# Optimization experiments

Hardware: AMD Instinct MI355X
Metric: run time of the kernel (lower is better)

## Reference

```python
import jax, jax.numpy as jnp
import numpy as np
import math

N_HEADS = 8
Q_DIM = 512          # number of query tokens (first Q_DIM rows of q)
INPUT_DIM = 512
EMBED_DIM = 512
HEAD_DIM = EMBED_DIM // N_HEADS  # key_dim == val_dim == 64
BATCH = 8
TOTAL_TOKENS = 4096  # Q_DIM queries + 3584 context tokens
NORM = 1.0 / math.sqrt(HEAD_DIM)


def setup_inputs() -> dict:
    key = jax.random.key(0)
    k1, k2, k3, k4, k5 = jax.random.split(key, 5)
    stdv = 1.0 / math.sqrt(HEAD_DIM)
    return {
        "q": jax.random.normal(k1, (BATCH, TOTAL_TOKENS, INPUT_DIM), dtype=jnp.float32),
        "W_query": jax.random.uniform(k2, (N_HEADS, INPUT_DIM, HEAD_DIM), minval=-stdv, maxval=stdv, dtype=jnp.float32),
        "W_key": jax.random.uniform(k3, (N_HEADS, INPUT_DIM, HEAD_DIM), minval=-stdv, maxval=stdv, dtype=jnp.float32),
        "W_val": jax.random.uniform(k4, (N_HEADS, INPUT_DIM, HEAD_DIM), minval=-stdv, maxval=stdv, dtype=jnp.float32),
        "W_out": jax.random.uniform(k5, (N_HEADS, HEAD_DIM, EMBED_DIM), minval=-1.0 / math.sqrt(EMBED_DIM), maxval=1.0 / math.sqrt(EMBED_DIM), dtype=jnp.float32),
    }


def reference(q, W_query, W_key, W_val, W_out):
    # Split packed input: first Q_DIM tokens are queries, rest are context.
    q_ = q[:, :Q_DIM, :]          # [b, nq, d_in]
    h = q[:, Q_DIM:, :]           # [b, g, d_in]
    Q = jnp.einsum('bqi,hik->hbqk', q_, W_query)   # [h, b, nq, dk]
    K = jnp.einsum('bgi,hik->hbgk', h, W_key)      # [h, b, g, dk]
    V = jnp.einsum('bgi,hiv->hbgv', h, W_val)      # [h, b, g, dv]
    compat = NORM * jnp.einsum('hbqk,hbgk->hbqg', Q, K)  # [h, b, nq, g]
    attn = jax.nn.softmax(compat, axis=-1)
    heads = jnp.einsum('hbqg,hbgv->hbqv', attn, V)       # [h, b, nq, dv]
    out = jnp.einsum('hbqv,hve->bqe', heads, W_out)      # [b, nq, embed]
    return out
```

## Files before the change

### kernel.cpp

```cpp
#include <hip/hip_runtime.h>

typedef _Float16 f16;
typedef _Float16 f16x4 __attribute__((ext_vector_type(4)));
typedef _Float16 f16x8 __attribute__((ext_vector_type(8)));
typedef float    f32x4 __attribute__((ext_vector_type(4)));

#define MFMA(a,b,c) __builtin_amdgcn_mfma_f32_16x16x32_f16(a,b,c,0,0,0)

__device__ __forceinline__ void gld16(const void* g, void* l) {
  typedef __attribute__((address_space(1))) unsigned GU;
  typedef __attribute__((address_space(3))) unsigned LU;
  __builtin_amdgcn_global_load_lds((GU*)g, (LU*)l, 16, 0, 0);
}

__global__ __launch_bounds__(256) void conv_w(
    const float* __restrict__ Wq, const float* __restrict__ Wk,
    const float* __restrict__ Wv, const float* __restrict__ Wo,
    f16* __restrict__ Wqt, f16* __restrict__ Wkt, f16* __restrict__ Wvt,
    f16* __restrict__ Wot)
{
  int idx = blockIdx.x * 256 + threadIdx.x;
  int c = idx & 511, i = idx >> 9;
  int h = c >> 6, k = c & 63;
  int src = (h * 512 + i) * 64 + k;
  Wqt[c * 512 + i] = (f16)(Wq[src] * 0.125f);
  Wkt[c * 512 + i] = (f16)Wk[src];
  Wvt[c * 512 + i] = (f16)Wv[src];
  Wot[idx] = (f16)Wo[(idx & 511) * 512 + (idx >> 9)];
}

__global__ __launch_bounds__(256) void proj_kernel(
    const float* __restrict__ q,
    const f16* __restrict__ Wqt, const f16* __restrict__ Wkt, const f16* __restrict__ Wvt,
    f16* __restrict__ Qh, f16* __restrict__ Kh, f16* __restrict__ Vtb)
{
  __shared__ f16 Asl[2][4096];
  __shared__ f16 Bsl[2][4096];

  int bid = blockIdx.x;
  int mode, t;
  if (bid < 128)       { mode = 0; t = bid; }
  else if (bid < 1024) { mode = 1; t = bid - 128; }
  else                 { mode = 2; t = bid - 1024; }
  int rt = t >> 2, ct = t & 3;
  const f16* Wt = (mode == 0) ? Wqt : (mode == 1) ? Wkt : Wvt;

  int tid = threadIdx.x, l = tid & 63, w = tid >> 6;
  int m0 = rt * 128, n0 = ct * 128;
  int wr = w >> 1, wc = w & 1;

  int arl = tid >> 3;
  int acol = (tid & 7) * 4;
  int agrow[4], awb[4];
#pragma unroll
  for (int p = 0; p < 4; ++p) {
    int m = m0 + p * 32 + arl;
    int grow;
    if (mode == 0) grow = (m >> 9) * 4096 + (m & 511);
    else { int b = m / 3584; grow = b * 4096 + 512 + (m - b * 3584); }
    agrow[p] = grow * 512;
    int r = p * 32 + arl, cg = tid & 7;
    awb[p] = r * 64 + (((cg >> 1) ^ (r & 3)) << 4) + (cg & 1) * 8;
  }
  int bn[2], bco[2];
#pragma unroll
  for (int j = 0; j < 2; ++j) {
    int n = (w * 2 + j) * 16 + (l >> 2);
    bn[j] = n;
    bco[j] = ((l & 3) ^ (n & 3)) * 8;
  }

  const f32x4 z4 = {0.f, 0.f, 0.f, 0.f};
  f32x4 acc[4][4];
#pragma unroll
  for (int i = 0; i < 4; ++i)
#pragma unroll
    for (int jj = 0; jj < 4; ++jj) acc[i][jj] = z4;

  f32x4 areg[4];
  auto aload = [&](int k0) {
#pragma unroll
    for (int p = 0; p < 4; ++p)
      areg[p] = *(const f32x4*)(q + agrow[p] + k0 + acol);
  };
  auto bstage = [&](int bufi, int k0) {
#pragma unroll
    for (int j = 0; j < 2; ++j)
      gld16(Wt + (n0 + bn[j]) * 512 + k0 + bco[j], &Bsl[bufi][(w * 2 + j) * 512]);
  };
  auto awrite = [&](int bufi) {
#pragma unroll
    for (int p = 0; p < 4; ++p) {
      f16x4 h4;
      h4[0] = (f16)areg[p][0]; h4[1] = (f16)areg[p][1];
      h4[2] = (f16)areg[p][2]; h4[3] = (f16)areg[p][3];
      *(f16x4*)((char*)&Asl[bufi][0] + awb[p]) = h4;
    }
  };

  aload(0); bstage(0, 0); awrite(0);
  __syncthreads();

  for (int ks = 0; ks < 16; ++ks) {
    int bufi = ks & 1;
    if (ks < 15) { aload((ks + 1) * 32); bstage(bufi ^ 1, (ks + 1) * 32); }
    const char* AB = (const char*)&Asl[bufi][0];
    const char* BB = (const char*)&Bsl[bufi][0];
    f16x8 af[4], bf[4];
#pragma unroll
    for (int mi = 0; mi < 4; ++mi) {
      int row = wr * 64 + mi * 16 + (l & 15);
      af[mi] = *(const f16x8*)(AB + row * 64 + (((l >> 4) ^ (row & 3)) << 4));
    }
#pragma unroll
    for (int ni = 0; ni < 4; ++ni) {
      int rn = wc * 64 + ni * 16 + (l & 15);
      bf[ni] = *(const f16x8*)(BB + rn * 64 + (((l >> 4) ^ (rn & 3)) << 4));
    }
#pragma unroll
    for (int mi = 0; mi < 4; ++mi)
#pragma unroll
      for (int ni = 0; ni < 4; ++ni)
        acc[mi][ni] = MFMA(af[mi], bf[ni], acc[mi][ni]);
    if (ks < 15) awrite(bufi ^ 1);
    __syncthreads();
  }

  if (mode < 2) {
    f16* Out = (mode == 0) ? Qh : Kh;
#pragma unroll
    for (int mi = 0; mi < 4; ++mi) {
      int row = m0 + wr * 64 + mi * 16 + (l >> 4) * 4;
#pragma unroll
      for (int ni = 0; ni < 4; ++ni) {
        int col = n0 + wc * 64 + ni * 16 + (l & 15);
#pragma unroll
        for (int r = 0; r < 4; ++r)
          Out[(row + r) * 512 + col] = (f16)acc[mi][ni][r];
      }
    }
  } else {
#pragma unroll
    for (int mi = 0; mi < 4; ++mi) {
      int m = m0 + wr * 64 + mi * 16 + (l >> 4) * 4;
      int b = m / 3584, g = m - b * 3584;
#pragma unroll
      for (int ni = 0; ni < 4; ++ni) {
        int c = n0 + wc * 64 + ni * 16 + (l & 15);
        int hh = c >> 6, v = c & 63;
        f16x4 o4;
        o4[0] = (f16)acc[mi][ni][0]; o4[1] = (f16)acc[mi][ni][1];
        o4[2] = (f16)acc[mi][ni][2]; o4[3] = (f16)acc[mi][ni][3];
        *(f16x4*)(Vtb + ((b * 8 + hh) * 64 + v) * 3584 + g) = o4;
      }
    }
  }
}

__global__ __launch_bounds__(512) void attn_kernel(
    const f16* __restrict__ Qh, const f16* __restrict__ Kh,
    const f16* __restrict__ Vtb, f16* __restrict__ Hm)
{
  __shared__ f16 Klds[2][4096];
  __shared__ f16 Vlds[2][4096];
  __shared__ f16 Plds[8192];

  int bid = blockIdx.x;
  int qt = bid & 3, h = (bid >> 2) & 7, bb = bid >> 5;
  int q0 = qt * 128;
  int tid = threadIdx.x, l = tid & 63, w = tid >> 6;

  f16x8 qf0, qf1;
  {
    int qrow = q0 + w * 16 + (l & 15);
    const f16* qb = Qh + (bb * 512 + qrow) * 512 + h * 64 + ((l >> 4) * 8);
    qf0 = *(const f16x8*)qb;
    qf1 = *(const f16x8*)(qb + 32);
  }

  bool isK = (w < 4);
  int sdo[2], ssrc[2];
#pragma unroll
  for (int j = 0; j < 2; ++j) {
    int id = (isK ? w : (w - 4)) * 2 + j;
    int rr = id * 8 + (l >> 3);
    int co = ((l & 7) ^ (rr & 7)) * 8;
    sdo[j] = id * 512;
    if (isK) ssrc[j] = (bb * 3584 + rr) * 512 + h * 64 + co;
    else     ssrc[j] = ((bb * 8 + h) * 64 + rr) * 3584 + co;
  }

  const f32x4 z4 = {0.f, 0.f, 0.f, 0.f};
  f32x4 acco[4];
#pragma unroll
  for (int i = 0; i < 4; ++i) acco[i] = z4;
  float mrow[4], lrow[4];
#pragma unroll
  for (int r = 0; r < 4; ++r) { mrow[r] = -1e30f; lrow[r] = 0.f; }

  char* PwB = (char*)&Plds[w * 1024];

  if (isK) { gld16(Kh + ssrc[0], &Klds[0][sdo[0]]); gld16(Kh + ssrc[1], &Klds[0][sdo[1]]); }
  else     { gld16(Vtb + ssrc[0], &Vlds[0][sdo[0]]); gld16(Vtb + ssrc[1], &Vlds[0][sdo[1]]); }
  __syncthreads();

  int buf = 0;
  for (int it = 0; it < 56; ++it) {
    if (it < 55) {
      int g0 = (it + 1) * 64;
      if (isK) { gld16(Kh + ssrc[0] + g0 * 512, &Klds[buf ^ 1][sdo[0]]);
                 gld16(Kh + ssrc[1] + g0 * 512, &Klds[buf ^ 1][sdo[1]]); }
      else     { gld16(Vtb + ssrc[0] + g0, &Vlds[buf ^ 1][sdo[0]]);
                 gld16(Vtb + ssrc[1] + g0, &Vlds[buf ^ 1][sdo[1]]); }
    }
    const char* KB = (const char*)&Klds[buf][0];
    const char* VB = (const char*)&Vlds[buf][0];

    f32x4 accs[4];
#pragma unroll
    for (int i = 0; i < 4; ++i) accs[i] = z4;
#pragma unroll
    for (int ni = 0; ni < 4; ++ni) {
      int g = ni * 16 + (l & 15);
      f16x8 kb0 = *(const f16x8*)(KB + g * 128 + ((((l >> 4)    ) ^ (g & 7)) << 4));
      f16x8 kb1 = *(const f16x8*)(KB + g * 128 + (((4 + (l >> 4)) ^ (g & 7)) << 4));
      accs[ni] = MFMA(qf0, kb0, accs[ni]);
      accs[ni] = MFMA(qf1, kb1, accs[ni]);
    }

    float alpha[4];
#pragma unroll
    for (int r = 0; r < 4; ++r) {
      float tm = fmaxf(fmaxf(accs[0][r], accs[1][r]), fmaxf(accs[2][r], accs[3][r]));
      tm = fmaxf(tm, __shfl_xor(tm, 1));
      tm = fmaxf(tm, __shfl_xor(tm, 2));
      tm = fmaxf(tm, __shfl_xor(tm, 4));
      tm = fmaxf(tm, __shfl_xor(tm, 8));
      float mn = fmaxf(mrow[r], tm);
      alpha[r] = __expf(mrow[r] - mn);
      mrow[r] = mn;
    }
    float rsum[4] = {0.f, 0.f, 0.f, 0.f};
    int qbase = (l >> 4) * 4;
#pragma unroll
    for (int ni = 0; ni < 4; ++ni) {
      int g = ni * 16 + (l & 15);
#pragma unroll
      for (int r = 0; r < 4; ++r) {
        float p = __expf(accs[ni][r] - mrow[r]);
        rsum[r] += p;
        int qq = qbase + r;
        *(f16*)(PwB + qq * 128 + ((((g >> 3) ^ (qq & 7))) << 4) + (g & 7) * 2) = (f16)p;
      }
    }
#pragma unroll
    for (int r = 0; r < 4; ++r) {
      rsum[r] += __shfl_xor(rsum[r], 1);
      rsum[r] += __shfl_xor(rsum[r], 2);
      rsum[r] += __shfl_xor(rsum[r], 4);
      rsum[r] += __shfl_xor(rsum[r], 8);
      lrow[r] = lrow[r] * alpha[r] + rsum[r];
    }
#pragma unroll
    for (int ni = 0; ni < 4; ++ni)
#pragma unroll
      for (int r = 0; r < 4; ++r) acco[ni][r] *= alpha[r];

    asm volatile("s_waitcnt lgkmcnt(0)" ::: "memory");

#pragma unroll
    for (int kc = 0; kc < 2; ++kc) {
      int qq = l & 15;
      int ch = kc * 4 + (l >> 4);
      f16x8 pa = *(const f16x8*)(PwB + qq * 128 + ((ch ^ (qq & 7)) << 4));
#pragma unroll
      for (int ni = 0; ni < 4; ++ni) {
        int v = ni * 16 + (l & 15);
        f16x8 vb = *(const f16x8*)(VB + v * 128 + ((ch ^ (v & 7)) << 4));
        acco[ni] = MFMA(pa, vb, acco[ni]);
      }
    }

    __syncthreads();
    buf ^= 1;
  }

#pragma unroll
  for (int r = 0; r < 4; ++r) {
    float inv = 1.f / lrow[r];
    int qrow = q0 + w * 16 + (l >> 4) * 4 + r;
    f16* ob = Hm + (bb * 512 + qrow) * 512 + h * 64 + (l & 15);
#pragma unroll
    for (int ni = 0; ni < 4; ++ni)
      ob[ni * 16] = (f16)(acco[ni][r] * inv);
  }
}

__global__ __launch_bounds__(256) void outproj_kernel(
    const f16* __restrict__ Hm, const f16* __restrict__ Wot, float* __restrict__ out)
{
  __shared__ f16 Asl[2][4096];
  __shared__ f16 Bsl[2][4096];
  int bid = blockIdx.x;
  int rt = bid >> 2, ct = bid & 3;
  int tid = threadIdx.x, l = tid & 63, w = tid >> 6;
  int m0 = rt * 128, n0 = ct * 128;
  int wr = w >> 1, wc = w & 1;

  int an[2], aco[2];
#pragma unroll
  for (int j = 0; j < 2; ++j) {
    int r = (w * 2 + j) * 16 + (l >> 2);
    an[j] = r;
    aco[j] = ((l & 3) ^ (r & 3)) * 8;
  }

  const f32x4 z4 = {0.f, 0.f, 0.f, 0.f};
  f32x4 acc[4][4];
#pragma unroll
  for (int i = 0; i < 4; ++i)
#pragma unroll
    for (int jj = 0; jj < 4; ++jj) acc[i][jj] = z4;

  auto stage = [&](int bufi, int k0) {
#pragma unroll
    for (int j = 0; j < 2; ++j) {
      gld16(Hm  + (m0 + an[j]) * 512 + k0 + aco[j], &Asl[bufi][(w * 2 + j) * 512]);
      gld16(Wot + (n0 + an[j]) * 512 + k0 + aco[j], &Bsl[bufi][(w * 2 + j) * 512]);
    }
  };

  stage(0, 0);
  __syncthreads();
  for (int ks = 0; ks < 16; ++ks) {
    int bufi = ks & 1;
    if (ks < 15) stage(bufi ^ 1, (ks + 1) * 32);
    const char* AB = (const char*)&Asl[bufi][0];
    const char* BB = (const char*)&Bsl[bufi][0];
    f16x8 af[4], bf[4];
#pragma unroll
    for (int mi = 0; mi < 4; ++mi) {
      int row = wr * 64 + mi * 16 + (l & 15);
      af[mi] = *(const f16x8*)(AB + row * 64 + (((l >> 4) ^ (row & 3)) << 4));
    }
#pragma unroll
    for (int ni = 0; ni < 4; ++ni) {
      int rn = wc * 64 + ni * 16 + (l & 15);
      bf[ni] = *(const f16x8*)(BB + rn * 64 + (((l >> 4) ^ (rn & 3)) << 4));
    }
#pragma unroll
    for (int mi = 0; mi < 4; ++mi)
#pragma unroll
      for (int ni = 0; ni < 4; ++ni)
        acc[mi][ni] = MFMA(af[mi], bf[ni], acc[mi][ni]);
    __syncthreads();
  }

#pragma unroll
  for (int mi = 0; mi < 4; ++mi) {
    int row = m0 + wr * 64 + mi * 16 + (l >> 4) * 4;
#pragma unroll
    for (int ni = 0; ni < 4; ++ni) {
      int col = n0 + wc * 64 + ni * 16 + (l & 15);
#pragma unroll
      for (int r = 0; r < 4; ++r)
        out[(row + r) * 512 + col] = acc[mi][ni][r];
    }
  }
}

extern "C" void kernel_launch(void* const* d_in, const int* in_sizes, int n_in,
                              void* d_out, int out_size, void* d_ws, size_t ws_size,
                              hipStream_t stream) {
  const float* q  = (const float*)d_in[0];
  const float* Wq = (const float*)d_in[1];
  const float* Wk = (const float*)d_in[2];
  const float* Wv = (const float*)d_in[3];
  const float* Wo = (const float*)d_in[4];
  float* out = (float*)d_out;

  f16* ws  = (f16*)d_ws;
  f16* Wqt = ws;
  f16* Wkt = Wqt + 262144;
  f16* Wvt = Wkt + 262144;
  f16* Wot = Wvt + 262144;
  f16* Qh  = Wot + 262144;
  f16* Kh  = Qh  + 4096 * 512;
  f16* Vtb = Kh  + 28672 * 512;
  f16* Hm  = Vtb + 28672 * 512;

  conv_w<<<dim3(1024), dim3(256), 0, stream>>>(Wq, Wk, Wv, Wo, Wqt, Wkt, Wvt, Wot);
  proj_kernel<<<dim3(1920), dim3(256), 0, stream>>>(q, Wqt, Wkt, Wvt, Qh, Kh, Vtb);
  attn_kernel<<<dim3(256), dim3(512), 0, stream>>>(Qh, Kh, Vtb, Hm);
  outproj_kernel<<<dim3(128), dim3(256), 0, stream>>>(Hm, Wot, out);
}
```

Before: 284.8 us.

## Split attention over two KV segments with merge kernel, exp2 softmax, tiled weight transpose

The attention kernel now splits the 3584 context tokens into two halves per block, doubling the grid to 512 blocks, and writes partial outputs plus row max and sum. A new merge kernel combines them. The change also swaps the MFMA operand order so each lane owns a single query row, which cuts cross-lane reductions. It uses exp2 with log2(e) folded into the query weights, and replaces the weight conversion with an LDS-tiled transpose. The goal is better CU occupancy on a 256-CU part and cheaper softmax, at the cost of an extra kernel launch and extra partial-output memory traffic.

```diff
diff --git a/kernel.cpp b/kernel.cpp
--- a/kernel.cpp
+++ b/kernel.cpp
@@ -7,26 +7,51 @@
 
 #define MFMA(a,b,c) __builtin_amdgcn_mfma_f32_16x16x32_f16(a,b,c,0,0,0)
 
+#if __has_builtin(__builtin_amdgcn_exp2f)
+#define EXP2(x) __builtin_amdgcn_exp2f(x)
+#else
+#define EXP2(x) exp2f(x)
+#endif
+
 __device__ __forceinline__ void gld16(const void* g, void* l) {
   typedef __attribute__((address_space(1))) unsigned GU;
   typedef __attribute__((address_space(3))) unsigned LU;
   __builtin_amdgcn_global_load_lds((GU*)g, (LU*)l, 16, 0, 0);
 }
 
-__global__ __launch_bounds__(256) void conv_w(
+__global__ __launch_bounds__(256) void transp_w(
     const float* __restrict__ Wq, const float* __restrict__ Wk,
     const float* __restrict__ Wv, const float* __restrict__ Wo,
     f16* __restrict__ Wqt, f16* __restrict__ Wkt, f16* __restrict__ Wvt,
     f16* __restrict__ Wot)
 {
-  int idx = blockIdx.x * 256 + threadIdx.x;
-  int c = idx & 511, i = idx >> 9;
-  int h = c >> 6, k = c & 63;
-  int src = (h * 512 + i) * 64 + k;
-  Wqt[c * 512 + i] = (f16)(Wq[src] * 0.125f);
-  Wkt[c * 512 + i] = (f16)Wk[src];
-  Wvt[c * 512 + i] = (f16)Wv[src];
-  Wot[idx] = (f16)Wo[(idx & 511) * 512 + (idx >> 9)];
+  __shared__ float T[64 * 65];
+  int bid = blockIdx.x, t = threadIdx.x;
+  int mat = bid >> 6;
+  int i0 = (bid & 7) * 64, c0 = ((bid >> 3) & 7) * 64;
+  const float* src; f16* dst; float scale = 1.f;
+  if      (mat == 0) { src = Wq; dst = Wqt; scale = 0.125f * 1.4426950408889634f; }
+  else if (mat == 1) { src = Wk; dst = Wkt; }
+  else if (mat == 2) { src = Wv; dst = Wvt; }
+  else               { src = Wo; dst = Wot; }
+#pragma unroll
+  for (int p = 0; p < 4; ++p) {
+    int row = p * 16 + (t >> 4), col = (t & 15) * 4;
+    const float* a = (mat < 3)
+        ? src + ((c0 >> 6) * 512 + i0 + row) * 64 + col
+        : src + (i0 + row) * 512 + c0 + col;
+    f32x4 v = *(const f32x4*)a;
+    T[row * 65 + col + 0] = v[0] * scale;
+    T[row * 65 + col + 1] = v[1] * scale;
+    T[row * 65 + col + 2] = v[2] * scale;
+    T[row * 65 + col + 3] = v[3] * scale;
+  }
+  __syncthreads();
+#pragma unroll
+  for (int p = 0; p < 16; ++p) {
+    int cc = (t >> 6) * 16 + p, ii = t & 63;
+    dst[(c0 + cc) * 512 + i0 + ii] = (f16)T[ii * 65 + cc];
+  }
 }
 
 __global__ __launch_bounds__(256) void proj_kernel(
@@ -157,16 +182,17 @@
   }
 }
 
-__global__ __launch_bounds__(512) void attn_kernel(
+__global__ __launch_bounds__(512, 4) void attn_kernel(
     const f16* __restrict__ Qh, const f16* __restrict__ Kh,
-    const f16* __restrict__ Vtb, f16* __restrict__ Hm)
+    const f16* __restrict__ Vtb, f16* __restrict__ Opart,
+    float* __restrict__ Ml, float* __restrict__ Ll)
 {
   __shared__ f16 Klds[2][4096];
   __shared__ f16 Vlds[2][4096];
-  __shared__ f16 Plds[8192];
+  __shared__ f16 Plds[8 * 1152];
 
   int bid = blockIdx.x;
-  int qt = bid & 3, h = (bid >> 2) & 7, bb = bid >> 5;
+  int seg = bid & 1, qt = (bid >> 1) & 3, h = (bid >> 3) & 7, bb = bid >> 6;
   int q0 = qt * 128;
   int tid = threadIdx.x, l = tid & 63, w = tid >> 6;
 
@@ -186,27 +212,27 @@
     int rr = id * 8 + (l >> 3);
     int co = ((l & 7) ^ (rr & 7)) * 8;
     sdo[j] = id * 512;
-    if (isK) ssrc[j] = (bb * 3584 + rr) * 512 + h * 64 + co;
-    else     ssrc[j] = ((bb * 8 + h) * 64 + rr) * 3584 + co;
+    if (isK) ssrc[j] = (bb * 3584 + seg * 1792 + rr) * 512 + h * 64 + co;
+    else     ssrc[j] = ((bb * 8 + h) * 64 + rr) * 3584 + seg * 1792 + co;
   }
 
   const f32x4 z4 = {0.f, 0.f, 0.f, 0.f};
   f32x4 acco[4];
 #pragma unroll
   for (int i = 0; i < 4; ++i) acco[i] = z4;
-  float mrow[4], lrow[4];
-#pragma unroll
-  for (int r = 0; r < 4; ++r) { mrow[r] = -1e30f; lrow[r] = 0.f; }
-
-  char* PwB = (char*)&Plds[w * 1024];
+  float mrow = -1e30f, lrow = 0.f;
+
+  char* PwB = (char*)&Plds[w * 1152];
+  int pwbase = (l & 15) * 144 + (l >> 4) * 8;
+  int prbase = (l & 15) * 144 + (l >> 4) * 16;
 
   if (isK) { gld16(Kh + ssrc[0], &Klds[0][sdo[0]]); gld16(Kh + ssrc[1], &Klds[0][sdo[1]]); }
   else     { gld16(Vtb + ssrc[0], &Vlds[0][sdo[0]]); gld16(Vtb + ssrc[1], &Vlds[0][sdo[1]]); }
   __syncthreads();
 
   int buf = 0;
-  for (int it = 0; it < 56; ++it) {
-    if (it < 55) {
+  for (int it = 0; it < 28; ++it) {
+    if (it < 27) {
       int g0 = (it + 1) * 64;
       if (isK) { gld16(Kh + ssrc[0] + g0 * 512, &Klds[buf ^ 1][sdo[0]]);
                  gld16(Kh + ssrc[1] + g0 * 512, &Klds[buf ^ 1][sdo[1]]); }
@@ -222,62 +248,54 @@
 #pragma unroll
     for (int ni = 0; ni < 4; ++ni) {
       int g = ni * 16 + (l & 15);
-      f16x8 kb0 = *(const f16x8*)(KB + g * 128 + ((((l >> 4)    ) ^ (g & 7)) << 4));
-      f16x8 kb1 = *(const f16x8*)(KB + g * 128 + (((4 + (l >> 4)) ^ (g & 7)) << 4));
-      accs[ni] = MFMA(qf0, kb0, accs[ni]);
-      accs[ni] = MFMA(qf1, kb1, accs[ni]);
-    }
-
-    float alpha[4];
-#pragma unroll
-    for (int r = 0; r < 4; ++r) {
-      float tm = fmaxf(fmaxf(accs[0][r], accs[1][r]), fmaxf(accs[2][r], accs[3][r]));
-      tm = fmaxf(tm, __shfl_xor(tm, 1));
-      tm = fmaxf(tm, __shfl_xor(tm, 2));
-      tm = fmaxf(tm, __shfl_xor(tm, 4));
-      tm = fmaxf(tm, __shfl_xor(tm, 8));
-      float mn = fmaxf(mrow[r], tm);
-      alpha[r] = __expf(mrow[r] - mn);
-      mrow[r] = mn;
-    }
-    float rsum[4] = {0.f, 0.f, 0.f, 0.f};
-    int qbase = (l >> 4) * 4;
+      const char* rp = KB + g * 128;
+      f16x8 k0 = *(const f16x8*)(rp + ((((l >> 4)    ) ^ (g & 7)) << 4));
+      f16x8 k1 = *(const f16x8*)(rp + (((4 + (l >> 4)) ^ (g & 7)) << 4));
+      accs[ni] = MFMA(k0, qf0, accs[ni]);
+      accs[ni] = MFMA(k1, qf1, accs[ni]);
+    }
+
+    float n0 = fmaxf(fmaxf(accs[0][0], accs[0][1]), fmaxf(accs[0][2], accs[0][3]));
+    float n1 = fmaxf(fmaxf(accs[1][0], accs[1][1]), fmaxf(accs[1][2], accs[1][3]));
+    float n2 = fmaxf(fmaxf(accs[2][0], accs[2][1]), fmaxf(accs[2][2], accs[2][3]));
+    float n3 = fmaxf(fmaxf(accs[3][0], accs[3][1]), fmaxf(accs[3][2], accs[3][3]));
+    float tm = fmaxf(fmaxf(n0, n1), fmaxf(n2, n3));
+    tm = fmaxf(tm, __shfl_xor(tm, 16));
+    tm = fmaxf(tm, __shfl_xor(tm, 32));
+    float mn = fmaxf(mrow, tm);
+    float alpha = EXP2(mrow - mn);
+    mrow = mn;
+
+    float rs = 0.f;
 #pragma unroll
     for (int ni = 0; ni < 4; ++ni) {
-      int g = ni * 16 + (l & 15);
-#pragma unroll
-      for (int r = 0; r < 4; ++r) {
-        float p = __expf(accs[ni][r] - mrow[r]);
-        rsum[r] += p;
-        int qq = qbase + r;
-        *(f16*)(PwB + qq * 128 + ((((g >> 3) ^ (qq & 7))) << 4) + (g & 7) * 2) = (f16)p;
-      }
-    }
-#pragma unroll
-    for (int r = 0; r < 4; ++r) {
-      rsum[r] += __shfl_xor(rsum[r], 1);
-      rsum[r] += __shfl_xor(rsum[r], 2);
-      rsum[r] += __shfl_xor(rsum[r], 4);
-      rsum[r] += __shfl_xor(rsum[r], 8);
-      lrow[r] = lrow[r] * alpha[r] + rsum[r];
-    }
+      float s0 = EXP2(accs[ni][0] - mrow);
+      float s1 = EXP2(accs[ni][1] - mrow);
+      float s2 = EXP2(accs[ni][2] - mrow);
+      float s3 = EXP2(accs[ni][3] - mrow);
+      rs += (s0 + s1) + (s2 + s3);
+      f16x4 p4;
+      p4[0] = (f16)s0; p4[1] = (f16)s1; p4[2] = (f16)s2; p4[3] = (f16)s3;
+      *(f16x4*)(PwB + pwbase + ni * 32) = p4;
+    }
+    rs += __shfl_xor(rs, 16);
+    rs += __shfl_xor(rs, 32);
+    lrow = lrow * alpha + rs;
 #pragma unroll
     for (int ni = 0; ni < 4; ++ni)
 #pragma unroll
-      for (int r = 0; r < 4; ++r) acco[ni][r] *= alpha[r];
+      for (int r = 0; r < 4; ++r) acco[ni][r] *= alpha;
 
     asm volatile("s_waitcnt lgkmcnt(0)" ::: "memory");
 
 #pragma unroll
     for (int kc = 0; kc < 2; ++kc) {
-      int qq = l & 15;
-      int ch = kc * 4 + (l >> 4);
-      f16x8 pa = *(const f16x8*)(PwB + qq * 128 + ((ch ^ (qq & 7)) << 4));
+      f16x8 pf = *(const f16x8*)(PwB + prbase + kc * 64);
 #pragma unroll
       for (int ni = 0; ni < 4; ++ni) {
         int v = ni * 16 + (l & 15);
-        f16x8 vb = *(const f16x8*)(VB + v * 128 + ((ch ^ (v & 7)) << 4));
-        acco[ni] = MFMA(pa, vb, acco[ni]);
+        f16x8 vf = *(const f16x8*)(VB + v * 128 + (((kc * 4 + (l >> 4)) ^ (v & 7)) << 4));
+        acco[ni] = MFMA(vf, pf, acco[ni]);
       }
     }
 
@@ -285,15 +303,39 @@
     buf ^= 1;
   }
 
-#pragma unroll
-  for (int r = 0; r < 4; ++r) {
-    float inv = 1.f / lrow[r];
-    int qrow = q0 + w * 16 + (l >> 4) * 4 + r;
-    f16* ob = Hm + (bb * 512 + qrow) * 512 + h * 64 + (l & 15);
-#pragma unroll
-    for (int ni = 0; ni < 4; ++ni)
-      ob[ni * 16] = (f16)(acco[ni][r] * inv);
-  }
+  float inv = 1.f / lrow;
+  int q = q0 + w * 16 + (l & 15);
+  size_t obase = ((size_t)(seg * 64 + bb * 8 + h) * 512 + q) * 64;
+#pragma unroll
+  for (int ni = 0; ni < 4; ++ni) {
+    f16x4 o4;
+    o4[0] = (f16)(acco[ni][0] * inv); o4[1] = (f16)(acco[ni][1] * inv);
+    o4[2] = (f16)(acco[ni][2] * inv); o4[3] = (f16)(acco[ni][3] * inv);
+    *(f16x4*)(Opart + obase + ni * 16 + (l >> 4) * 4) = o4;
+  }
+  if ((l >> 4) == 0) {
+    int mi = (seg * 64 + bb * 8 + h) * 512 + q;
+    Ml[mi] = mrow; Ll[mi] = lrow;
+  }
+}
+
+__global__ __launch_bounds__(256) void merge_kernel(
+    const f16* __restrict__ Opart, const float* __restrict__ Ml,
+    const float* __restrict__ Ll, f16* __restrict__ Hm)
+{
+  int row = blockIdx.x * 4 + (threadIdx.x >> 6);
+  int l = threadIdx.x & 63;
+  int bh = row >> 9, q = row & 511;
+  int i0 = bh * 512 + q;
+  int i1 = (64 + bh) * 512 + q;
+  float o0 = (float)Opart[(size_t)i0 * 64 + l];
+  float o1 = (float)Opart[(size_t)i1 * 64 + l];
+  float m0 = Ml[i0], l0 = Ll[i0], m1 = Ml[i1], l1 = Ll[i1];
+  float m = fmaxf(m0, m1);
+  float w0 = EXP2(m0 - m) * l0, w1 = EXP2(m1 - m) * l1;
+  float o = (w0 * o0 + w1 * o1) / (w0 + w1);
+  int bb = bh >> 3, hh = bh & 7;
+  Hm[((size_t)(bb * 512 + q)) * 512 + hh * 64 + l] = (f16)o;
 }
 
 __global__ __launch_bounds__(256) void outproj_kernel(
@@ -387,10 +429,14 @@
   f16* Qh  = Wot + 262144;
   f16* Kh  = Qh  + 4096 * 512;
   f16* Vtb = Kh  + 28672 * 512;
-  f16* Hm  = Vtb + 28672 * 512;
-
-  conv_w<<<dim3(1024), dim3(256), 0, stream>>>(Wq, Wk, Wv, Wo, Wqt, Wkt, Wvt, Wot);
+  f16* Opart = Vtb + 28672 * 512;
+  float* Ml = (float*)(Opart + 2 * 64 * 512 * 64);
+  float* Ll = Ml + 65536;
+  f16* Hm = Qh;
+
+  transp_w<<<dim3(256),  dim3(256), 0, stream>>>(Wq, Wk, Wv, Wo, Wqt, Wkt, Wvt, Wot);
   proj_kernel<<<dim3(1920), dim3(256), 0, stream>>>(q, Wqt, Wkt, Wvt, Qh, Kh, Vtb);
-  attn_kernel<<<dim3(256), dim3(512), 0, stream>>>(Qh, Kh, Vtb, Hm);
+  attn_kernel<<<dim3(512), dim3(512), 0, stream>>>(Qh, Kh, Vtb, Opart, Ml, Ll);
+  merge_kernel<<<dim3(8192), dim3(256), 0, stream>>>(Opart, Ml, Ll, Hm);
   outproj_kernel<<<dim3(128), dim3(256), 0, stream>>>(Hm, Wot, out);
 }
```

After: 243.1 us. -14.7%, faster.
